# Performance work log

Measured on AMD Instinct MI355X. Metric: run time of the kernel, lower is better.

The kernel has to match this reference:

```python
import jax, jax.numpy as jnp
import numpy as np

B, DIM, T, SIZE = 32, 128, 4096, 512


def setup_inputs() -> dict:
    key = jax.random.key(0)
    k1, k2 = jax.random.split(key)
    H = jax.random.normal(k1, (B, DIM, T), dtype=jnp.float32)
    # nn.init.uniform_ -> U[0, 1)
    units = jax.random.uniform(k2, (DIM, SIZE), dtype=jnp.float32)
    return {"H": H, "units": units}


def reference(H, units):
    # H: (B, dim, T), units: (dim, size)
    Ht = jnp.swapaxes(H, 1, 2)  # (B, T, dim)
    # squared L2 distance via expansion: ||h||^2 - 2 h.m + ||m||^2  -> (B, T, size)
    h2 = jnp.sum(Ht * Ht, axis=-1, keepdims=True)          # (B, T, 1)
    m2 = jnp.sum(units * units, axis=0)                    # (size,)
    cross = jnp.einsum('btd,ds->bts', Ht, units)           # (B, T, size)
    sqdist = h2 - 2.0 * cross + m2                         # (B, T, size)
    # exp(-d^2) / sum over memory units == softmax(-d^2) along size axis
    C = jax.nn.softmax(-sqdist, axis=-1)                   # (B, T, size)
    return jnp.swapaxes(C, 1, 2)                           # (B, size, T)
```

## Files before the change

### kernel.cpp

```cpp
#include <hip/hip_runtime.h>
#include <cstddef>

constexpr int kB  = 32;
constexpr int kD  = 128;
constexpr int kT  = 4096;
constexpr int kS  = 512;
constexpr int kMT = 32;
constexpr int kLsStride = 516;

typedef __attribute__((ext_vector_type(8))) short bf16x8;
typedef __attribute__((ext_vector_type(4))) float f32x4;

__device__ __forceinline__ void split_bf16(float x, short& hi, short& lo) {
    union { float f; unsigned u; } a; a.f = x;
    unsigned r = (a.u + 0x7FFFu + ((a.u >> 16) & 1u)) & 0xFFFF0000u;
    union { unsigned u; float f; } h; h.u = r;
    hi = (short)(r >> 16);
    float res = x - h.f;
    union { float f; unsigned u; } c; c.f = res;
    lo = (short)((c.u + 0x7FFFu + ((c.u >> 16) & 1u)) >> 16);
}

__global__ void prep_kernel(const float* __restrict__ units,
                            short* __restrict__ Bhi, short* __restrict__ Blo,
                            float* __restrict__ m2) {
    const int blk = blockIdx.x, tid = threadIdx.x;
    if (blk < 256) {
        int idx  = blk * 256 + tid;
        int j    = idx & 7;
        int lane = (idx >> 3) & 63;
        int kk   = (idx >> 9) & 3;
        int nt   = idx >> 11;
        int k = kk * 32 + (lane >> 4) * 8 + j;
        int n = nt * 16 + (lane & 15);
        float u = units[k * kS + n];
        short h, l; split_bf16(u, h, l);
        Bhi[idx] = h; Blo[idx] = l;
    } else {
        for (int s = tid; s < kS; s += 256) {
            float acc = 0.f;
#pragma unroll 8
            for (int d = 0; d < kD; ++d) {
                float u = units[d * kS + s];
                acc = fmaf(u, u, acc);
            }
            m2[s] = acc;
        }
    }
}

__global__ __launch_bounds__(256, 2)
void mb_mfma(const float* __restrict__ H,
             const short* __restrict__ Bhi, const short* __restrict__ Blo,
             const float* __restrict__ m2, float* __restrict__ out) {
    __shared__ float Ls[kMT][kLsStride];
    __shared__ float red[8 * 32];
    __shared__ float rowM[kMT];
    __shared__ float rowInv[kMT];

    const int tid  = threadIdx.x;
    const int wave = tid >> 6;
    const int lane = tid & 63;
    const int q    = lane >> 4;
    const int nl   = lane & 15;
    const int t0   = blockIdx.x * kMT;
    const int b    = blockIdx.y;

    bf16x8 Ahi[2][4], Alo[2][4];
    {
        const float* Hb = H + ((size_t)b * kD) * kT + t0;
#pragma unroll
        for (int mt = 0; mt < 2; ++mt) {
            const int m = mt * 16 + nl;
#pragma unroll
            for (int kk = 0; kk < 4; ++kk) {
#pragma unroll
                for (int j = 0; j < 8; ++j) {
                    float x = Hb[(size_t)(kk * 32 + q * 8 + j) * kT + m];
                    short h, l; split_bf16(x, h, l);
                    Ahi[mt][kk][j] = h;
                    Alo[mt][kk][j] = l;
                }
            }
        }
    }

#pragma unroll
    for (int np = 0; np < 4; ++np) {
        const int ntA = wave * 8 + np * 2;
        const int ntB = ntA + 1;
        f32x4 accA0 = {0.f, 0.f, 0.f, 0.f}, accA1 = {0.f, 0.f, 0.f, 0.f};
        f32x4 accB0 = {0.f, 0.f, 0.f, 0.f}, accB1 = {0.f, 0.f, 0.f, 0.f};
#pragma unroll
        for (int kk = 0; kk < 4; ++kk) {
            const int baseA = ((ntA * 4 + kk) * 64 + lane) * 8;
            const int baseB = ((ntB * 4 + kk) * 64 + lane) * 8;
            bf16x8 BhA = *(const bf16x8*)(Bhi + baseA);
            bf16x8 BlA = *(const bf16x8*)(Blo + baseA);
            bf16x8 BhB = *(const bf16x8*)(Bhi + baseB);
            bf16x8 BlB = *(const bf16x8*)(Blo + baseB);
            accA0 = __builtin_amdgcn_mfma_f32_16x16x32_bf16(Ahi[0][kk], BhA, accA0, 0, 0, 0);
            accA1 = __builtin_amdgcn_mfma_f32_16x16x32_bf16(Ahi[1][kk], BhA, accA1, 0, 0, 0);
            accB0 = __builtin_amdgcn_mfma_f32_16x16x32_bf16(Ahi[0][kk], BhB, accB0, 0, 0, 0);
            accB1 = __builtin_amdgcn_mfma_f32_16x16x32_bf16(Ahi[1][kk], BhB, accB1, 0, 0, 0);
            accA0 = __builtin_amdgcn_mfma_f32_16x16x32_bf16(Alo[0][kk], BhA, accA0, 0, 0, 0);
            accA1 = __builtin_amdgcn_mfma_f32_16x16x32_bf16(Alo[1][kk], BhA, accA1, 0, 0, 0);
            accB0 = __builtin_amdgcn_mfma_f32_16x16x32_bf16(Alo[0][kk], BhB, accB0, 0, 0, 0);
            accB1 = __builtin_amdgcn_mfma_f32_16x16x32_bf16(Alo[1][kk], BhB, accB1, 0, 0, 0);
            accA0 = __builtin_amdgcn_mfma_f32_16x16x32_bf16(Ahi[0][kk], BlA, accA0, 0, 0, 0);
            accA1 = __builtin_amdgcn_mfma_f32_16x16x32_bf16(Ahi[1][kk], BlA, accA1, 0, 0, 0);
            accB0 = __builtin_amdgcn_mfma_f32_16x16x32_bf16(Ahi[0][kk], BlB, accB0, 0, 0, 0);
            accB1 = __builtin_amdgcn_mfma_f32_16x16x32_bf16(Ahi[1][kk], BlB, accB1, 0, 0, 0);
        }
        const float m2A = m2[ntA * 16 + nl];
        const float m2B = m2[ntB * 16 + nl];
#pragma unroll
        for (int r = 0; r < 4; ++r) {
            Ls[q * 4 + r     ][ntA * 16 + nl] = fmaf(2.f, accA0[r], -m2A);
            Ls[q * 4 + r + 16][ntA * 16 + nl] = fmaf(2.f, accA1[r], -m2A);
            Ls[q * 4 + r     ][ntB * 16 + nl] = fmaf(2.f, accB0[r], -m2B);
            Ls[q * 4 + r + 16][ntB * 16 + nl] = fmaf(2.f, accB1[r], -m2B);
        }
    }
    __syncthreads();

    const int r  = tid & 31;
    const int jc = tid >> 5;
    float* Lrow = &Ls[r][jc * 64];
    float mx = -3.0e38f;
#pragma unroll 8
    for (int k = 0; k < 64; ++k) mx = fmaxf(mx, Lrow[k]);
    red[jc * 32 + r] = mx;
    __syncthreads();
    if (tid < 32) {
        float m = red[tid];
#pragma unroll
        for (int k = 1; k < 8; ++k) m = fmaxf(m, red[k * 32 + tid]);
        rowM[tid] = m;
    }
    __syncthreads();
    const float M = rowM[r];
    float ssum = 0.f;
#pragma unroll 4
    for (int k = 0; k < 64; ++k) {
        float e = __expf(Lrow[k] - M);
        Lrow[k] = e;
        ssum += e;
    }
    red[jc * 32 + r] = ssum;
    __syncthreads();
    if (tid < 32) {
        float s = 0.f;
#pragma unroll
        for (int k = 0; k < 8; ++k) s += red[k * 32 + tid];
        rowInv[tid] = 1.f / s;
    }
    __syncthreads();

    const int i4    = (tid & 7) * 4;
    const int sBase = tid >> 3;
    const float inv0 = rowInv[i4 + 0];
    const float inv1 = rowInv[i4 + 1];
    const float inv2 = rowInv[i4 + 2];
    const float inv3 = rowInv[i4 + 3];
    float* outB = out + ((size_t)b * kS) * kT + t0;
#pragma unroll
    for (int w = 0; w < 16; ++w) {
        int s = sBase + w * 32;
        f32x4 v;
        v[0] = Ls[i4 + 0][s] * inv0;
        v[1] = Ls[i4 + 1][s] * inv1;
        v[2] = Ls[i4 + 2][s] * inv2;
        v[3] = Ls[i4 + 3][s] * inv3;
        __builtin_nontemporal_store(v, (f32x4*)(outB + (size_t)s * kT + i4));
    }
}

extern "C" void kernel_launch(void* const* d_in, const int* in_sizes, int n_in,
                              void* d_out, int out_size, void* d_ws, size_t ws_size,
                              hipStream_t stream) {
    const float* H     = (const float*)d_in[0];
    const float* units = (const float*)d_in[1];
    float* out = (float*)d_out;

    char* ws = (char*)d_ws;
    short* Bhi = (short*)ws;
    short* Blo = (short*)(ws + 131072);
    float* m2  = (float*)(ws + 262144);

    prep_kernel<<<dim3(257), dim3(256), 0, stream>>>(units, Bhi, Blo, m2);
    dim3 grid(kT / kMT, kB);
    mb_mfma<<<grid, dim3(256), 0, stream>>>(H, Bhi, Blo, m2, out);
}
```

Measured before the change: 391.2 us.

## Keep softmax in registers, stage A via LDS, shrink LDS for higher occupancy

```diff
diff --git a/kernel.cpp b/kernel.cpp
--- a/kernel.cpp
+++ b/kernel.cpp
@@ -6,7 +6,6 @@
 constexpr int kT  = 4096;
 constexpr int kS  = 512;
 constexpr int kMT = 32;
-constexpr int kLsStride = 516;
 
 typedef __attribute__((ext_vector_type(8))) short bf16x8;
 typedef __attribute__((ext_vector_type(4))) float f32x4;
@@ -49,12 +48,18 @@
     }
 }
 
-__global__ __launch_bounds__(256, 2)
+constexpr int kAStr = 136;
+constexpr int kLStr = 132;
+
+__global__ __launch_bounds__(256, 4)
 void mb_mfma(const float* __restrict__ H,
              const short* __restrict__ Bhi, const short* __restrict__ Blo,
              const float* __restrict__ m2, float* __restrict__ out) {
-    __shared__ float Ls[kMT][kLsStride];
-    __shared__ float red[8 * 32];
+    __shared__ __align__(16) union SMem {
+        struct { short hi[kMT * kAStr]; short lo[kMT * kAStr]; } a;
+        float ls[kMT * kLStr];
+    } sm;
+    __shared__ float redBuf[128];
     __shared__ float rowM[kMT];
     __shared__ float rowInv[kMT];
 
@@ -65,114 +70,152 @@
     const int nl   = lane & 15;
     const int t0   = blockIdx.x * kMT;
     const int b    = blockIdx.y;
-
-    bf16x8 Ahi[2][4], Alo[2][4];
+    const float* Hb = H + ((size_t)b * kD) * kT + t0;
+
     {
-        const float* Hb = H + ((size_t)b * kD) * kT + t0;
+        const int ms = tid & 31;
+        const int kb = tid >> 5;
+#pragma unroll
+        for (int half = 0; half < 2; ++half) {
+            const int k0 = (kb + half * 8) * 8;
+            bf16x8 vh, vl;
+#pragma unroll
+            for (int j = 0; j < 8; ++j) {
+                float x = Hb[(size_t)(k0 + j) * kT + ms];
+                short h, l; split_bf16(x, h, l);
+                vh[j] = h; vl[j] = l;
+            }
+            *(bf16x8*)(sm.a.hi + ms * kAStr + k0) = vh;
+            *(bf16x8*)(sm.a.lo + ms * kAStr + k0) = vl;
+        }
+    }
+    __syncthreads();
+
+    f32x4 acc[8][2];
+#pragma unroll
+    for (int n8 = 0; n8 < 8; ++n8)
+#pragma unroll
+        for (int mt = 0; mt < 2; ++mt)
+            acc[n8][mt] = (f32x4){0.f, 0.f, 0.f, 0.f};
+
+#pragma unroll
+    for (int kk = 0; kk < 4; ++kk) {
+        bf16x8 Ah[2], Al[2];
 #pragma unroll
         for (int mt = 0; mt < 2; ++mt) {
-            const int m = mt * 16 + nl;
-#pragma unroll
-            for (int kk = 0; kk < 4; ++kk) {
-#pragma unroll
-                for (int j = 0; j < 8; ++j) {
-                    float x = Hb[(size_t)(kk * 32 + q * 8 + j) * kT + m];
-                    short h, l; split_bf16(x, h, l);
-                    Ahi[mt][kk][j] = h;
-                    Alo[mt][kk][j] = l;
-                }
+            const int off = (mt * 16 + nl) * kAStr + kk * 32 + q * 8;
+            Ah[mt] = *(const bf16x8*)(sm.a.hi + off);
+            Al[mt] = *(const bf16x8*)(sm.a.lo + off);
+        }
+#pragma unroll
+        for (int n8 = 0; n8 < 8; ++n8) {
+            const int nt = n8 * 4 + wave;
+            const int base = ((nt * 4 + kk) * 64 + lane) * 8;
+            bf16x8 Bh = *(const bf16x8*)(Bhi + base);
+            bf16x8 Bl = *(const bf16x8*)(Blo + base);
+            acc[n8][0] = __builtin_amdgcn_mfma_f32_16x16x32_bf16(Ah[0], Bh, acc[n8][0], 0, 0, 0);
+            acc[n8][1] = __builtin_amdgcn_mfma_f32_16x16x32_bf16(Ah[1], Bh, acc[n8][1], 0, 0, 0);
+            acc[n8][0] = __builtin_amdgcn_mfma_f32_16x16x32_bf16(Al[0], Bh, acc[n8][0], 0, 0, 0);
+            acc[n8][1] = __builtin_amdgcn_mfma_f32_16x16x32_bf16(Al[1], Bh, acc[n8][1], 0, 0, 0);
+            acc[n8][0] = __builtin_amdgcn_mfma_f32_16x16x32_bf16(Ah[0], Bl, acc[n8][0], 0, 0, 0);
+            acc[n8][1] = __builtin_amdgcn_mfma_f32_16x16x32_bf16(Ah[1], Bl, acc[n8][1], 0, 0, 0);
+        }
+    }
+
+    float m2v[8];
+#pragma unroll
+    for (int n8 = 0; n8 < 8; ++n8) m2v[n8] = m2[(n8 * 4 + wave) * 16 + nl];
+#pragma unroll
+    for (int n8 = 0; n8 < 8; ++n8)
+#pragma unroll
+        for (int mt = 0; mt < 2; ++mt)
+#pragma unroll
+            for (int r = 0; r < 4; ++r)
+                acc[n8][mt][r] = fmaf(2.f, acc[n8][mt][r], -m2v[n8]);
+
+#pragma unroll
+    for (int mt = 0; mt < 2; ++mt)
+#pragma unroll
+        for (int r = 0; r < 4; ++r) {
+            float v = acc[0][mt][r];
+#pragma unroll
+            for (int n8 = 1; n8 < 8; ++n8) v = fmaxf(v, acc[n8][mt][r]);
+            v = fmaxf(v, __shfl_xor(v, 1, 16));
+            v = fmaxf(v, __shfl_xor(v, 2, 16));
+            v = fmaxf(v, __shfl_xor(v, 4, 16));
+            v = fmaxf(v, __shfl_xor(v, 8, 16));
+            if (nl == 0) redBuf[wave * 32 + mt * 16 + q * 4 + r] = v;
+        }
+    __syncthreads();
+    if (tid < kMT) {
+        float v = redBuf[tid];
+#pragma unroll
+        for (int w = 1; w < 4; ++w) v = fmaxf(v, redBuf[w * 32 + tid]);
+        rowM[tid] = v;
+    }
+    __syncthreads();
+
+#pragma unroll
+    for (int mt = 0; mt < 2; ++mt)
+#pragma unroll
+        for (int r = 0; r < 4; ++r) {
+            const float M = rowM[mt * 16 + q * 4 + r];
+            float s = 0.f;
+#pragma unroll
+            for (int n8 = 0; n8 < 8; ++n8) {
+                float e = __expf(acc[n8][mt][r] - M);
+                acc[n8][mt][r] = e;
+                s += e;
             }
-        }
-    }
-
-#pragma unroll
-    for (int np = 0; np < 4; ++np) {
-        const int ntA = wave * 8 + np * 2;
-        const int ntB = ntA + 1;
-        f32x4 accA0 = {0.f, 0.f, 0.f, 0.f}, accA1 = {0.f, 0.f, 0.f, 0.f};
-        f32x4 accB0 = {0.f, 0.f, 0.f, 0.f}, accB1 = {0.f, 0.f, 0.f, 0.f};
-#pragma unroll
-        for (int kk = 0; kk < 4; ++kk) {
-            const int baseA = ((ntA * 4 + kk) * 64 + lane) * 8;
-            const int baseB = ((ntB * 4 + kk) * 64 + lane) * 8;
-            bf16x8 BhA = *(const bf16x8*)(Bhi + baseA);
-            bf16x8 BlA = *(const bf16x8*)(Blo + baseA);
-            bf16x8 BhB = *(const bf16x8*)(Bhi + baseB);
-            bf16x8 BlB = *(const bf16x8*)(Blo + baseB);
-            accA0 = __builtin_amdgcn_mfma_f32_16x16x32_bf16(Ahi[0][kk], BhA, accA0, 0, 0, 0);
-            accA1 = __builtin_amdgcn_mfma_f32_16x16x32_bf16(Ahi[1][kk], BhA, accA1, 0, 0, 0);
-            accB0 = __builtin_amdgcn_mfma_f32_16x16x32_bf16(Ahi[0][kk], BhB, accB0, 0, 0, 0);
-            accB1 = __builtin_amdgcn_mfma_f32_16x16x32_bf16(Ahi[1][kk], BhB, accB1, 0, 0, 0);
-            accA0 = __builtin_amdgcn_mfma_f32_16x16x32_bf16(Alo[0][kk], BhA, accA0, 0, 0, 0);
-            accA1 = __builtin_amdgcn_mfma_f32_16x16x32_bf16(Alo[1][kk], BhA, accA1, 0, 0, 0);
-            accB0 = __builtin_amdgcn_mfma_f32_16x16x32_bf16(Alo[0][kk], BhB, accB0, 0, 0, 0);
-            accB1 = __builtin_amdgcn_mfma_f32_16x16x32_bf16(Alo[1][kk], BhB, accB1, 0, 0, 0);
-            accA0 = __builtin_amdgcn_mfma_f32_16x16x32_bf16(Ahi[0][kk], BlA, accA0, 0, 0, 0);
-            accA1 = __builtin_amdgcn_mfma_f32_16x16x32_bf16(Ahi[1][kk], BlA, accA1, 0, 0, 0);
-            accB0 = __builtin_amdgcn_mfma_f32_16x16x32_bf16(Ahi[0][kk], BlB, accB0, 0, 0, 0);
-            accB1 = __builtin_amdgcn_mfma_f32_16x16x32_bf16(Ahi[1][kk], BlB, accB1, 0, 0, 0);
-        }
-        const float m2A = m2[ntA * 16 + nl];
-        const float m2B = m2[ntB * 16 + nl];
+            s += __shfl_xor(s, 1, 16);
+            s += __shfl_xor(s, 2, 16);
+            s += __shfl_xor(s, 4, 16);
+            s += __shfl_xor(s, 8, 16);
+            if (nl == 0) redBuf[wave * 32 + mt * 16 + q * 4 + r] = s;
+        }
+    __syncthreads();
+    if (tid < kMT) {
+        float s = redBuf[tid] + redBuf[32 + tid] + redBuf[64 + tid] + redBuf[96 + tid];
+        rowInv[tid] = 1.f / s;
+    }
+    __syncthreads();
+
+#pragma unroll
+    for (int mt = 0; mt < 2; ++mt)
 #pragma unroll
         for (int r = 0; r < 4; ++r) {
-            Ls[q * 4 + r     ][ntA * 16 + nl] = fmaf(2.f, accA0[r], -m2A);
-            Ls[q * 4 + r + 16][ntA * 16 + nl] = fmaf(2.f, accA1[r], -m2A);
-            Ls[q * 4 + r     ][ntB * 16 + nl] = fmaf(2.f, accB0[r], -m2B);
-            Ls[q * 4 + r + 16][ntB * 16 + nl] = fmaf(2.f, accB1[r], -m2B);
-        }
-    }
-    __syncthreads();
-
-    const int r  = tid & 31;
-    const int jc = tid >> 5;
-    float* Lrow = &Ls[r][jc * 64];
-    float mx = -3.0e38f;
-#pragma unroll 8
-    for (int k = 0; k < 64; ++k) mx = fmaxf(mx, Lrow[k]);
-    red[jc * 32 + r] = mx;
-    __syncthreads();
-    if (tid < 32) {
-        float m = red[tid];
-#pragma unroll
-        for (int k = 1; k < 8; ++k) m = fmaxf(m, red[k * 32 + tid]);
-        rowM[tid] = m;
-    }
-    __syncthreads();
-    const float M = rowM[r];
-    float ssum = 0.f;
-#pragma unroll 4
-    for (int k = 0; k < 64; ++k) {
-        float e = __expf(Lrow[k] - M);
-        Lrow[k] = e;
-        ssum += e;
-    }
-    red[jc * 32 + r] = ssum;
-    __syncthreads();
-    if (tid < 32) {
-        float s = 0.f;
-#pragma unroll
-        for (int k = 0; k < 8; ++k) s += red[k * 32 + tid];
-        rowInv[tid] = 1.f / s;
-    }
-    __syncthreads();
-
-    const int i4    = (tid & 7) * 4;
-    const int sBase = tid >> 3;
-    const float inv0 = rowInv[i4 + 0];
-    const float inv1 = rowInv[i4 + 1];
-    const float inv2 = rowInv[i4 + 2];
-    const float inv3 = rowInv[i4 + 3];
+            const float inv = rowInv[mt * 16 + q * 4 + r];
+#pragma unroll
+            for (int n8 = 0; n8 < 8; ++n8) acc[n8][mt][r] *= inv;
+        }
+
     float* outB = out + ((size_t)b * kS) * kT + t0;
-#pragma unroll
-    for (int w = 0; w < 16; ++w) {
-        int s = sBase + w * 32;
-        f32x4 v;
-        v[0] = Ls[i4 + 0][s] * inv0;
-        v[1] = Ls[i4 + 1][s] * inv1;
-        v[2] = Ls[i4 + 2][s] * inv2;
-        v[3] = Ls[i4 + 3][s] * inv3;
-        __builtin_nontemporal_store(v, (f32x4*)(outB + (size_t)s * kT + i4));
+    const int i4 = (tid & 7) * 4;
+    const int su = tid >> 3;
+#pragma unroll
+    for (int rnd = 0; rnd < 4; ++rnd) {
+        __syncthreads();
+#pragma unroll
+        for (int h = 0; h < 2; ++h) {
+            const int n8 = rnd * 2 + h;
+            const int sl = h * 64 + wave * 16 + nl;
+#pragma unroll
+            for (int mt = 0; mt < 2; ++mt)
+#pragma unroll
+                for (int r = 0; r < 4; ++r)
+                    sm.ls[(mt * 16 + q * 4 + r) * kLStr + sl] = acc[n8][mt][r];
+        }
+        __syncthreads();
+#pragma unroll
+        for (int p = 0; p < 4; ++p) {
+            const int sl = su + p * 32;
+            f32x4 v;
+            v[0] = sm.ls[(i4 + 0) * kLStr + sl];
+            v[1] = sm.ls[(i4 + 1) * kLStr + sl];
+            v[2] = sm.ls[(i4 + 2) * kLStr + sl];
+            v[3] = sm.ls[(i4 + 3) * kLStr + sl];
+            __builtin_nontemporal_store(v, (f32x4*)(outB + (size_t)(rnd * 128 + sl) * kT + i4));
+        }
     }
 }
 
```

New measurement: 373.8 us. 4.4% less time.
